# Kernel optimization log

Measured on AMD Instinct MI355X. Metric: run time of the kernel, lower is better.

The kernel has to match this reference:

```python
import jax, jax.numpy as jnp
import numpy as np

N_NODES = 100000
N_EDGES = 1600000
D = 64  # input_dim = hidden_dim = output_dim
EPS = 1e-12


def _sage_layer(x, src, dst, wl, bl, wr, br):
    # gather messages from source nodes: [E, D]
    msg = x[src]
    # scatter-mean onto destination nodes
    s = jax.ops.segment_sum(msg, dst, num_segments=x.shape[0])
    cnt = jax.ops.segment_sum(jnp.ones((src.shape[0], 1), x.dtype), dst, num_segments=x.shape[0])
    prop = s / jnp.maximum(cnt, 1.0)
    out = x @ wl.T + bl + prop @ wr.T + br
    # F.normalize(out, p=2, dim=1)
    norm = jnp.sqrt(jnp.sum(out * out, axis=1, keepdims=True))
    return out / jnp.maximum(norm, EPS)


def setup_inputs() -> dict:
    key = jax.random.key(0)
    ks = jax.random.split(key, 12)
    d = D

    def lin(k, fan_in, fan_out):
        bound = 1.0 / np.sqrt(fan_in)
        kw, kb = jax.random.split(k)
        w = jax.random.uniform(kw, (fan_out, fan_in), jnp.float32, -bound, bound)
        b = jax.random.uniform(kb, (fan_out,), jnp.float32, -bound, bound)
        return w, b

    x = jax.random.normal(ks[0], (N_NODES, d), jnp.float32)
    edge_index = jax.random.randint(ks[1], (2, N_EDGES), 0, N_NODES, jnp.int64)

    w1l, b1l = lin(ks[2], d, d)
    w1r, b1r = lin(ks[3], d, d)
    w2l, b2l = lin(ks[4], d, d)
    w2r, b2r = lin(ks[5], d, d)
    wp1, bp1 = lin(ks[6], d, d)
    wp2, bp2 = lin(ks[7], d, d)

    return {"x": x, "edge_index": edge_index,
            "w1l": w1l, "b1l": b1l, "w1r": w1r, "b1r": b1r,
            "w2l": w2l, "b2l": b2l, "w2r": w2r, "b2r": b2r,
            "wp1": wp1, "bp1": bp1, "wp2": wp2, "bp2": bp2}


def reference(x, edge_index, w1l, b1l, w1r, b1r, w2l, b2l, w2r, b2r, wp1, bp1, wp2, bp2):
    src = edge_index[0]
    dst = edge_index[1]
    # layer 1: GraphSage -> relu (dropout is identity in eval)
    h = _sage_layer(x, src, dst, w1l, b1l, w1r, b1r)
    h = jax.nn.relu(h)
    # layer 2
    h = _sage_layer(h, src, dst, w2l, b2l, w2r, b2r)
    h = jax.nn.relu(h)
    # post_mp: Linear -> Dropout(identity) -> Linear; emb=True so no log_softmax
    h = h @ wp1.T + bp1
    h = h @ wp2.T + bp2
    return h
```

## Files before the change

kernel.cpp:

```cpp
#include <hip/hip_runtime.h>

#define NN 100000
#define NE 1600000
#define DD 64
#define NB 196
#define BKT 512
#define CAP 9000
#define NOCT 12500
#define NH 391
#define NG1 1024

__global__ void init_kernel(int* __restrict__ gcursor) {
  int t = threadIdx.x;
  if (t < NB) gcursor[t] = t * CAP;
}

__launch_bounds__(256)
__global__ void scatter2_kernel(const int* __restrict__ src, const int* __restrict__ dst,
                                int* __restrict__ gcursor, int2* __restrict__ pairs) {
  __shared__ int lh[NB];
  __shared__ int lbase[NB];
  __shared__ int lcur[NB];
  const int NQ = NE / 4;
  int t = blockIdx.x * 256 + threadIdx.x;
  const int nt = NH * 256;
  for (int i = threadIdx.x; i < NB; i += 256) lh[i] = 0;
  __syncthreads();
  int4 dv[4], sv[4];
  bool pv[4];
  #pragma unroll
  for (int k = 0; k < 4; ++k) {
    int idx = t + k * nt;
    pv[k] = idx < NQ;
    if (pv[k]) {
      dv[k] = reinterpret_cast<const int4*>(dst)[idx];
      sv[k] = reinterpret_cast<const int4*>(src)[idx];
      atomicAdd(&lh[dv[k].x >> 9], 1);
      atomicAdd(&lh[dv[k].y >> 9], 1);
      atomicAdd(&lh[dv[k].z >> 9], 1);
      atomicAdd(&lh[dv[k].w >> 9], 1);
    }
  }
  __syncthreads();
  for (int i = threadIdx.x; i < NB; i += 256) {
    lcur[i] = 0;
    lbase[i] = lh[i] ? atomicAdd(&gcursor[i], lh[i]) : 0;
  }
  __syncthreads();
  #pragma unroll
  for (int k = 0; k < 4; ++k) {
    if (pv[k]) {
      int b;
      b = dv[k].x >> 9; pairs[lbase[b] + atomicAdd(&lcur[b], 1)] = make_int2(sv[k].x, dv[k].x);
      b = dv[k].y >> 9; pairs[lbase[b] + atomicAdd(&lcur[b], 1)] = make_int2(sv[k].y, dv[k].y);
      b = dv[k].z >> 9; pairs[lbase[b] + atomicAdd(&lcur[b], 1)] = make_int2(sv[k].z, dv[k].z);
      b = dv[k].w >> 9; pairs[lbase[b] + atomicAdd(&lcur[b], 1)] = make_int2(sv[k].w, dv[k].w);
    }
  }
}

__launch_bounds__(256)
__global__ void csr_kernel(const int2* __restrict__ pairs, const int* __restrict__ gcursor,
                           int* __restrict__ deg, int* __restrict__ off,
                           int* __restrict__ adj) {
  __shared__ int lh[BKT];
  __shared__ int wsum[4];
  int b = blockIdx.x;
  int t = threadIdx.x;
  int rs = b * CAP, re = gcursor[b];
  lh[2 * t] = 0;
  lh[2 * t + 1] = 0;
  __syncthreads();
  for (int i = rs + t; i < re; i += 256)
    atomicAdd(&lh[pairs[i].y - b * BKT], 1);
  __syncthreads();
  int lane = t & 63, w = t >> 6;
  int h0 = lh[2 * t], h1 = lh[2 * t + 1];
  int s = h0 + h1, incl = s;
  #pragma unroll
  for (int o = 1; o < 64; o <<= 1) {
    int u = __shfl_up(incl, o, 64);
    if (lane >= o) incl += u;
  }
  if (lane == 63) wsum[w] = incl;
  __syncthreads();
  int prefix = 0;
  for (int u = 0; u < w; ++u) prefix += wsum[u];
  int excl = prefix + incl - s;
  int n0 = b * BKT + 2 * t, n1 = n0 + 1;
  if (n0 < NN) { deg[n0] = h0; off[n0] = rs + excl; }
  if (n1 < NN) { deg[n1] = h1; off[n1] = rs + excl + h0; }
  lh[2 * t] = excl;
  lh[2 * t + 1] = excl + h0;
  __syncthreads();
  for (int i = rs + t; i < re; i += 256) {
    int2 e = pairs[i];
    int pos = atomicAdd(&lh[e.y - b * BKT], 1);
    adj[rs + pos] = e.x;
  }
}

__launch_bounds__(256)
__global__ void selfgemm_kernel(const float* __restrict__ x,
                                const float* __restrict__ wl,
                                const float* __restrict__ bl,
                                const float* __restrict__ br,
                                float* __restrict__ tmp,
                                const float* __restrict__ wp1, const float* __restrict__ bp1,
                                const float* __restrict__ wp2, const float* __restrict__ bp2,
                                float* __restrict__ wc4f, float* __restrict__ bc) {
  __shared__ float4 wA4[16 * 64] __attribute__((aligned(16)));
  __shared__ float sp[4][8][DD] __attribute__((aligned(16)));
  int bid = blockIdx.x;
  if (bid < NG1) {
    int tid = threadIdx.x;
    int j = tid & 63;
    int w = tid >> 6;
    float* wAf = (float*)wA4;
    for (int i = tid; i < DD * DD; i += 256) {
      int jj = i >> 6, k = i & 63;
      wAf[(((k >> 2) * 64) + jj) * 4 + (k & 3)] = wl[i];
    }
    float bias = bl[j] + br[j];
    __syncthreads();
    const int ngrp = 3125;
    for (int grp = bid; grp < ngrp; grp += NG1) {
      int n0 = (grp * 4 + w) * 8;
      const float4* xg = reinterpret_cast<const float4*>(&x[(size_t)n0 * DD]);
      float4* spv = reinterpret_cast<float4*>(&sp[w][0][0]);
      spv[j] = xg[j];
      spv[j + 64] = xg[j + 64];
      float acc[8];
      #pragma unroll
      for (int i = 0; i < 8; ++i) acc[i] = bias;
      #pragma unroll
      for (int q = 0; q < 16; ++q) {
        int kb = q * 4;
        float4 wq = wA4[q * 64 + j];
        #pragma unroll
        for (int i = 0; i < 8; ++i) {
          float4 sv = *(const float4*)&sp[w][i][kb];
          float a = acc[i];
          a = fmaf(sv.x, wq.x, a);
          a = fmaf(sv.y, wq.y, a);
          a = fmaf(sv.z, wq.z, a);
          a = fmaf(sv.w, wq.w, a);
          acc[i] = a;
        }
      }
      #pragma unroll
      for (int i = 0; i < 8; ++i) tmp[(size_t)(n0 + i) * DD + j] = acc[i];
    }
  } else {
    int t = threadIdx.x;
    for (int idx = t; idx < DD * DD; idx += 256) {
      int jp = idx >> 6, k = idx & 63;
      float s = 0.f;
      #pragma unroll
      for (int m = 0; m < DD; ++m) s = fmaf(wp2[jp * DD + m], wp1[m * DD + k], s);
      wc4f[(((k >> 2) * 64) + jp) * 4 + (k & 3)] = s;
    }
    if (t < DD) {
      float s = bp2[t];
      #pragma unroll
      for (int m = 0; m < DD; ++m) s = fmaf(wp2[t * DD + m], bp1[m], s);
      bc[t] = s;
    }
  }
}

__launch_bounds__(256)
__global__ void gather_kernel(const float* __restrict__ x,
                              const int* __restrict__ off,
                              const int* __restrict__ deg,
                              const int* __restrict__ adj,
                              float* __restrict__ prop) {
  const float4* X = reinterpret_cast<const float4*>(x);
  int wid = (blockIdx.x * 256 + threadIdx.x) >> 6;
  int nwaves = (gridDim.x * 256) >> 6;
  int lane = threadIdx.x & 63;
  int g = lane >> 4;
  int s = lane & 15;
  const int NQUAD = NN / 4;
  for (int q = wid; q < NQUAD; q += nwaves) {
    int n = q * 4 + g;
    int start = off[n];
    int d = deg[n];
    float4 a0 = {0,0,0,0}, a1 = {0,0,0,0}, a2 = {0,0,0,0}, a3 = {0,0,0,0};
    int t = 0;
    for (; t + 4 <= d; t += 4) {
      int i0 = adj[start + t + 0];
      int i1 = adj[start + t + 1];
      int i2 = adj[start + t + 2];
      int i3 = adj[start + t + 3];
      float4 v0 = X[i0 * 16 + s];
      float4 v1 = X[i1 * 16 + s];
      float4 v2 = X[i2 * 16 + s];
      float4 v3 = X[i3 * 16 + s];
      a0.x += v0.x; a0.y += v0.y; a0.z += v0.z; a0.w += v0.w;
      a1.x += v1.x; a1.y += v1.y; a1.z += v1.z; a1.w += v1.w;
      a2.x += v2.x; a2.y += v2.y; a2.z += v2.z; a2.w += v2.w;
      a3.x += v3.x; a3.y += v3.y; a3.z += v3.z; a3.w += v3.w;
    }
    if (t < d) {
      int dm = d - 1;
      int u1 = (t + 1 < d) ? t + 1 : dm;
      int u2 = (t + 2 < d) ? t + 2 : dm;
      int i0 = adj[start + t];
      int i1 = adj[start + u1];
      int i2 = adj[start + u2];
      float4 v0 = X[i0 * 16 + s];
      float4 v1 = X[i1 * 16 + s];
      float4 v2 = X[i2 * 16 + s];
      a0.x += v0.x; a0.y += v0.y; a0.z += v0.z; a0.w += v0.w;
      if (t + 1 < d) { a1.x += v1.x; a1.y += v1.y; a1.z += v1.z; a1.w += v1.w; }
      if (t + 2 < d) { a2.x += v2.x; a2.y += v2.y; a2.z += v2.z; a2.w += v2.w; }
    }
    float rc = 1.0f / fmaxf((float)d, 1.0f);
    float4 r;
    r.x = ((a0.x + a1.x) + (a2.x + a3.x)) * rc;
    r.y = ((a0.y + a1.y) + (a2.y + a3.y)) * rc;
    r.z = ((a0.z + a1.z) + (a2.z + a3.z)) * rc;
    r.w = ((a0.w + a1.w) + (a2.w + a3.w)) * rc;
    reinterpret_cast<float4*>(prop)[n * 16 + s] = r;
  }
}

__launch_bounds__(512, 4)
__global__ void gemm_light_kernel(float* __restrict__ out,
                                  const float* __restrict__ prop,
                                  const float* __restrict__ wr) {
  __shared__ float4 wrA4[16 * 64] __attribute__((aligned(16)));
  __shared__ float pp[8][8][DD] __attribute__((aligned(16)));
  int tid = threadIdx.x;
  int j = tid & 63;
  int w = tid >> 6;
  float* wrf = (float*)wrA4;
  for (int i = tid; i < DD * DD; i += 512) {
    int jj = i >> 6, k = i & 63;
    wrf[(((k >> 2) * 64) + jj) * 4 + (k & 3)] = wr[i];
  }
  __syncthreads();

  const int ngrp = (NOCT + 7) / 8;
  for (int grp = blockIdx.x; grp < ngrp; grp += gridDim.x) {
    int o = grp * 8 + w;
    if (o >= NOCT) continue;
    int n0 = o * 8;

    const float4* pg = reinterpret_cast<const float4*>(&prop[(size_t)n0 * DD]);
    float4* ppv = reinterpret_cast<float4*>(&pp[w][0][0]);
    ppv[j] = pg[j];
    ppv[j + 64] = pg[j + 64];

    float acc[8];
    #pragma unroll
    for (int i = 0; i < 8; ++i) acc[i] = out[(size_t)(n0 + i) * DD + j];

    #pragma unroll
    for (int q = 0; q < 16; ++q) {
      int kb = q * 4;
      float4 wq = wrA4[q * 64 + j];
      #pragma unroll
      for (int i = 0; i < 8; ++i) {
        float4 pv = *(const float4*)&pp[w][i][kb];
        float a = acc[i];
        a = fmaf(pv.x, wq.x, a);
        a = fmaf(pv.y, wq.y, a);
        a = fmaf(pv.z, wq.z, a);
        a = fmaf(pv.w, wq.w, a);
        acc[i] = a;
      }
    }

    #pragma unroll
    for (int i = 0; i < 8; ++i) {
      float a = acc[i];
      float ss = a * a;
      #pragma unroll
      for (int o2 = 32; o2 > 0; o2 >>= 1) ss += __shfl_xor(ss, o2, 64);
      float ov = a / fmaxf(sqrtf(ss), 1e-12f);
      ov = fmaxf(ov, 0.0f);
      out[(size_t)(n0 + i) * DD + j] = ov;
    }
  }
}

__launch_bounds__(512, 4)
__global__ void sage_post_kernel(const float* __restrict__ xin,
                                 const float* __restrict__ prop,
                                 const float* __restrict__ wl,
                                 const float* __restrict__ bl,
                                 const float* __restrict__ wr,
                                 const float* __restrict__ br,
                                 const float4* __restrict__ wc4,
                                 const float* __restrict__ bc,
                                 float* __restrict__ out) {
  __shared__ float4 wlA4[16 * 64] __attribute__((aligned(16)));
  __shared__ float4 wrA4[16 * 64] __attribute__((aligned(16)));
  __shared__ float sp[8][8][DD] __attribute__((aligned(16)));
  __shared__ float pp[8][8][DD] __attribute__((aligned(16)));
  int tid = threadIdx.x;
  int j = tid & 63;
  int w = tid >> 6;

  float* wlf = (float*)wlA4;
  float* wrf = (float*)wrA4;
  for (int i = tid; i < DD * DD; i += 512) {
    int jj = i >> 6, k = i & 63;
    wlf[(((k >> 2) * 64) + jj) * 4 + (k & 3)] = wl[i];
    wrf[(((k >> 2) * 64) + jj) * 4 + (k & 3)] = wr[i];
  }
  float bias = bl[j] + br[j];
  float bcv = bc[j];
  __syncthreads();

  const int ngrp = (NOCT + 7) / 8;
  for (int grp = blockIdx.x; grp < ngrp; grp += gridDim.x) {
    int o = grp * 8 + w;
    if (o >= NOCT) continue;
    int n0 = o * 8;

    const float4* xg = reinterpret_cast<const float4*>(&xin[(size_t)n0 * DD]);
    const float4* pg = reinterpret_cast<const float4*>(&prop[(size_t)n0 * DD]);
    float4* spv = reinterpret_cast<float4*>(&sp[w][0][0]);
    float4* ppv = reinterpret_cast<float4*>(&pp[w][0][0]);
    spv[j] = xg[j];
    spv[j + 64] = xg[j + 64];
    ppv[j] = pg[j];
    ppv[j + 64] = pg[j + 64];

    float acc[8];
    #pragma unroll
    for (int i = 0; i < 8; ++i) acc[i] = bias;

    #pragma unroll
    for (int q = 0; q < 16; ++q) {
      int kb = q * 4;
      float4 wlq = wlA4[q * 64 + j];
      float4 wrq = wrA4[q * 64 + j];
      #pragma unroll
      for (int i = 0; i < 8; ++i) {
        float4 sv = *(const float4*)&sp[w][i][kb];
        float4 pv = *(const float4*)&pp[w][i][kb];
        float a = acc[i];
        a = fmaf(sv.x, wlq.x, a);
        a = fmaf(sv.y, wlq.y, a);
        a = fmaf(sv.z, wlq.z, a);
        a = fmaf(sv.w, wlq.w, a);
        a = fmaf(pv.x, wrq.x, a);
        a = fmaf(pv.y, wrq.y, a);
        a = fmaf(pv.z, wrq.z, a);
        a = fmaf(pv.w, wrq.w, a);
        acc[i] = a;
      }
    }

    #pragma unroll
    for (int i = 0; i < 8; ++i) {
      float a = acc[i];
      float ss = a * a;
      #pragma unroll
      for (int o2 = 32; o2 > 0; o2 >>= 1) ss += __shfl_xor(ss, o2, 64);
      float ov = a / fmaxf(sqrtf(ss), 1e-12f);
      ov = fmaxf(ov, 0.0f);
      sp[w][i][j] = ov;
    }

    float acc2[8];
    #pragma unroll
    for (int i = 0; i < 8; ++i) acc2[i] = bcv;
    #pragma unroll
    for (int q = 0; q < 16; ++q) {
      int kb = q * 4;
      float4 wq = wc4[q * 64 + j];
      #pragma unroll
      for (int i = 0; i < 8; ++i) {
        float4 hv = *(const float4*)&sp[w][i][kb];
        float a = acc2[i];
        a = fmaf(hv.x, wq.x, a);
        a = fmaf(hv.y, wq.y, a);
        a = fmaf(hv.z, wq.z, a);
        a = fmaf(hv.w, wq.w, a);
        acc2[i] = a;
      }
    }
    #pragma unroll
    for (int i = 0; i < 8; ++i) out[(size_t)(n0 + i) * DD + j] = acc2[i];
  }
}

extern "C" void kernel_launch(void* const* d_in, const int* in_sizes, int n_in,
                              void* d_out, int out_size, void* d_ws, size_t ws_size,
                              hipStream_t stream) {
  const float* x   = (const float*)d_in[0];
  const int*   ei  = (const int*)d_in[1];
  const float* w1l = (const float*)d_in[2];
  const float* b1l = (const float*)d_in[3];
  const float* w1r = (const float*)d_in[4];
  const float* b1r = (const float*)d_in[5];
  const float* w2l = (const float*)d_in[6];
  const float* b2l = (const float*)d_in[7];
  const float* w2r = (const float*)d_in[8];
  const float* b2r = (const float*)d_in[9];
  const float* wp1 = (const float*)d_in[10];
  const float* bp1 = (const float*)d_in[11];
  const float* wp2 = (const float*)d_in[12];
  const float* bp2 = (const float*)d_in[13];
  float* out = (float*)d_out;

  const int* src = ei;
  const int* dst = ei + NE;

  int* deg     = (int*)d_ws;
  int* off     = deg + 102400;
  int* aux     = off + 102400;
  int* gcursor = aux;
  float* wc4f  = (float*)(aux + 1024);
  float* bc    = wc4f + 4096;
  int* adj     = (int*)(bc + 1024);
  float* prop  = (float*)(adj + NB * CAP);
  int2* pairs  = (int2*)prop;

  init_kernel<<<1, 256, 0, stream>>>(gcursor);
  scatter2_kernel<<<NH, 256, 0, stream>>>(src, dst, gcursor, pairs);
  csr_kernel<<<NB, 256, 0, stream>>>(pairs, gcursor, deg, off, adj);

  selfgemm_kernel<<<NG1 + 1, 256, 0, stream>>>(x, w1l, b1l, b1r, out,
                                               wp1, bp1, wp2, bp2, wc4f, bc);

  gather_kernel<<<2048, 256, 0, stream>>>(x, off, deg, adj, prop);
  gemm_light_kernel<<<1024, 512, 0, stream>>>(out, prop, w1r);

  gather_kernel<<<2048, 256, 0, stream>>>(out, off, deg, adj, prop);
  sage_post_kernel<<<512, 512, 0, stream>>>(out, prop, w2l, b2l, w2r, b2r,
                                            (const float4*)wc4f, bc, out);
}
```

Measured before the change: 275.9 us.

## Fuse neighbor gather with per-layer GEMM and normalize kernels

Merges each layer's mean-aggregation gather kernel with the following dense transform, normalization and ReLU kernel. Each wave gathers four nodes into shared memory and immediately applies the weight matrices, so the intermediate prop buffer is never written to or read back from global memory. Layer 1 now writes to a separate h buffer, reading the self-term from out, and the second fused kernel reads h and writes the final output. In exchange, the gather's memory latency and the GEMM's arithmetic now run in the same wave, the GEMM tile shrinks from 8 to 4 rows, and the weight staging in shared memory may limit occupancy.

Measured after the change: 302.9 us. +9.8%, slower.

```diff
diff --git a/kernel.cpp b/kernel.cpp
--- a/kernel.cpp
+++ b/kernel.cpp
@@ -6,9 +6,9 @@
 #define NB 196
 #define BKT 512
 #define CAP 9000
-#define NOCT 12500
 #define NH 391
 #define NG1 1024
+#define NQUAD (NN / 4)
 
 __global__ void init_kernel(int* __restrict__ gcursor) {
   int t = threadIdx.x;
@@ -169,19 +169,31 @@
   }
 }
 
-__launch_bounds__(256)
-__global__ void gather_kernel(const float* __restrict__ x,
+__launch_bounds__(512)
+__global__ void fused1_kernel(const float* __restrict__ x,
                               const int* __restrict__ off,
                               const int* __restrict__ deg,
                               const int* __restrict__ adj,
-                              float* __restrict__ prop) {
+                              const float* __restrict__ tmp,
+                              const float* __restrict__ wr,
+                              float* __restrict__ h) {
+  __shared__ float4 wrA4[16 * 64] __attribute__((aligned(16)));
+  __shared__ float pp[8][4][DD] __attribute__((aligned(16)));
+  int tid = threadIdx.x;
+  int j = tid & 63;
+  int w = tid >> 6;
+  float* wrf = (float*)wrA4;
+  for (int i = tid; i < DD * DD; i += 512) {
+    int jj = i >> 6, k = i & 63;
+    wrf[(((k >> 2) * 64) + jj) * 4 + (k & 3)] = wr[i];
+  }
+  __syncthreads();
+
   const float4* X = reinterpret_cast<const float4*>(x);
-  int wid = (blockIdx.x * 256 + threadIdx.x) >> 6;
-  int nwaves = (gridDim.x * 256) >> 6;
-  int lane = threadIdx.x & 63;
-  int g = lane >> 4;
-  int s = lane & 15;
-  const int NQUAD = NN / 4;
+  int g = j >> 4;
+  int s = j & 15;
+  int wid = blockIdx.x * 8 + w;
+  int nwaves = gridDim.x * 8;
   for (int q = wid; q < NQUAD; q += nwaves) {
     int n = q * 4 + g;
     int start = off[n];
@@ -222,47 +234,18 @@
     r.y = ((a0.y + a1.y) + (a2.y + a3.y)) * rc;
     r.z = ((a0.z + a1.z) + (a2.z + a3.z)) * rc;
     r.w = ((a0.w + a1.w) + (a2.w + a3.w)) * rc;
-    reinterpret_cast<float4*>(prop)[n * 16 + s] = r;
-  }
-}
-
-__launch_bounds__(512, 4)
-__global__ void gemm_light_kernel(float* __restrict__ out,
-                                  const float* __restrict__ prop,
-                                  const float* __restrict__ wr) {
-  __shared__ float4 wrA4[16 * 64] __attribute__((aligned(16)));
-  __shared__ float pp[8][8][DD] __attribute__((aligned(16)));
-  int tid = threadIdx.x;
-  int j = tid & 63;
-  int w = tid >> 6;
-  float* wrf = (float*)wrA4;
-  for (int i = tid; i < DD * DD; i += 512) {
-    int jj = i >> 6, k = i & 63;
-    wrf[(((k >> 2) * 64) + jj) * 4 + (k & 3)] = wr[i];
-  }
-  __syncthreads();
-
-  const int ngrp = (NOCT + 7) / 8;
-  for (int grp = blockIdx.x; grp < ngrp; grp += gridDim.x) {
-    int o = grp * 8 + w;
-    if (o >= NOCT) continue;
-    int n0 = o * 8;
-
-    const float4* pg = reinterpret_cast<const float4*>(&prop[(size_t)n0 * DD]);
-    float4* ppv = reinterpret_cast<float4*>(&pp[w][0][0]);
-    ppv[j] = pg[j];
-    ppv[j + 64] = pg[j + 64];
-
-    float acc[8];
-    #pragma unroll
-    for (int i = 0; i < 8; ++i) acc[i] = out[(size_t)(n0 + i) * DD + j];
-
-    #pragma unroll
-    for (int q = 0; q < 16; ++q) {
-      int kb = q * 4;
-      float4 wq = wrA4[q * 64 + j];
-      #pragma unroll
-      for (int i = 0; i < 8; ++i) {
+    *(float4*)&pp[w][g][s * 4] = r;
+
+    int n0 = q * 4;
+    float acc[4];
+    #pragma unroll
+    for (int i = 0; i < 4; ++i) acc[i] = tmp[(size_t)(n0 + i) * DD + j];
+    #pragma unroll
+    for (int qq = 0; qq < 16; ++qq) {
+      int kb = qq * 4;
+      float4 wq = wrA4[qq * 64 + j];
+      #pragma unroll
+      for (int i = 0; i < 4; ++i) {
         float4 pv = *(const float4*)&pp[w][i][kb];
         float a = acc[i];
         a = fmaf(pv.x, wq.x, a);
@@ -272,38 +255,38 @@
         acc[i] = a;
       }
     }
-
-    #pragma unroll
-    for (int i = 0; i < 8; ++i) {
+    #pragma unroll
+    for (int i = 0; i < 4; ++i) {
       float a = acc[i];
       float ss = a * a;
       #pragma unroll
       for (int o2 = 32; o2 > 0; o2 >>= 1) ss += __shfl_xor(ss, o2, 64);
       float ov = a / fmaxf(sqrtf(ss), 1e-12f);
       ov = fmaxf(ov, 0.0f);
-      out[(size_t)(n0 + i) * DD + j] = ov;
-    }
-  }
-}
-
-__launch_bounds__(512, 4)
-__global__ void sage_post_kernel(const float* __restrict__ xin,
-                                 const float* __restrict__ prop,
-                                 const float* __restrict__ wl,
-                                 const float* __restrict__ bl,
-                                 const float* __restrict__ wr,
-                                 const float* __restrict__ br,
-                                 const float4* __restrict__ wc4,
-                                 const float* __restrict__ bc,
-                                 float* __restrict__ out) {
+      h[(size_t)(n0 + i) * DD + j] = ov;
+    }
+  }
+}
+
+__launch_bounds__(512)
+__global__ void fused2_kernel(const float* __restrict__ h,
+                              const int* __restrict__ off,
+                              const int* __restrict__ deg,
+                              const int* __restrict__ adj,
+                              const float* __restrict__ wl,
+                              const float* __restrict__ bl,
+                              const float* __restrict__ wr,
+                              const float* __restrict__ br,
+                              const float4* __restrict__ wc4,
+                              const float* __restrict__ bc,
+                              float* __restrict__ out) {
   __shared__ float4 wlA4[16 * 64] __attribute__((aligned(16)));
   __shared__ float4 wrA4[16 * 64] __attribute__((aligned(16)));
-  __shared__ float sp[8][8][DD] __attribute__((aligned(16)));
-  __shared__ float pp[8][8][DD] __attribute__((aligned(16)));
+  __shared__ float sp[8][4][DD] __attribute__((aligned(16)));
+  __shared__ float pp[8][4][DD] __attribute__((aligned(16)));
   int tid = threadIdx.x;
   int j = tid & 63;
   int w = tid >> 6;
-
   float* wlf = (float*)wlA4;
   float* wrf = (float*)wrA4;
   for (int i = tid; i < DD * DD; i += 512) {
@@ -315,32 +298,68 @@
   float bcv = bc[j];
   __syncthreads();
 
-  const int ngrp = (NOCT + 7) / 8;
-  for (int grp = blockIdx.x; grp < ngrp; grp += gridDim.x) {
-    int o = grp * 8 + w;
-    if (o >= NOCT) continue;
-    int n0 = o * 8;
-
-    const float4* xg = reinterpret_cast<const float4*>(&xin[(size_t)n0 * DD]);
-    const float4* pg = reinterpret_cast<const float4*>(&prop[(size_t)n0 * DD]);
+  const float4* X = reinterpret_cast<const float4*>(h);
+  int g = j >> 4;
+  int s = j & 15;
+  int wid = blockIdx.x * 8 + w;
+  int nwaves = gridDim.x * 8;
+  for (int q = wid; q < NQUAD; q += nwaves) {
+    int n = q * 4 + g;
+    int start = off[n];
+    int d = deg[n];
+    float4 a0 = {0,0,0,0}, a1 = {0,0,0,0}, a2 = {0,0,0,0}, a3 = {0,0,0,0};
+    int t = 0;
+    for (; t + 4 <= d; t += 4) {
+      int i0 = adj[start + t + 0];
+      int i1 = adj[start + t + 1];
+      int i2 = adj[start + t + 2];
+      int i3 = adj[start + t + 3];
+      float4 v0 = X[i0 * 16 + s];
+      float4 v1 = X[i1 * 16 + s];
+      float4 v2 = X[i2 * 16 + s];
+      float4 v3 = X[i3 * 16 + s];
+      a0.x += v0.x; a0.y += v0.y; a0.z += v0.z; a0.w += v0.w;
+      a1.x += v1.x; a1.y += v1.y; a1.z += v1.z; a1.w += v1.w;
+      a2.x += v2.x; a2.y += v2.y; a2.z += v2.z; a2.w += v2.w;
+      a3.x += v3.x; a3.y += v3.y; a3.z += v3.z; a3.w += v3.w;
+    }
+    if (t < d) {
+      int dm = d - 1;
+      int u1 = (t + 1 < d) ? t + 1 : dm;
+      int u2 = (t + 2 < d) ? t + 2 : dm;
+      int i0 = adj[start + t];
+      int i1 = adj[start + u1];
+      int i2 = adj[start + u2];
+      float4 v0 = X[i0 * 16 + s];
+      float4 v1 = X[i1 * 16 + s];
+      float4 v2 = X[i2 * 16 + s];
+      a0.x += v0.x; a0.y += v0.y; a0.z += v0.z; a0.w += v0.w;
+      if (t + 1 < d) { a1.x += v1.x; a1.y += v1.y; a1.z += v1.z; a1.w += v1.w; }
+      if (t + 2 < d) { a2.x += v2.x; a2.y += v2.y; a2.z += v2.z; a2.w += v2.w; }
+    }
+    float rc = 1.0f / fmaxf((float)d, 1.0f);
+    float4 r;
+    r.x = ((a0.x + a1.x) + (a2.x + a3.x)) * rc;
+    r.y = ((a0.y + a1.y) + (a2.y + a3.y)) * rc;
+    r.z = ((a0.z + a1.z) + (a2.z + a3.z)) * rc;
+    r.w = ((a0.w + a1.w) + (a2.w + a3.w)) * rc;
+    *(float4*)&pp[w][g][s * 4] = r;
+
+    int n0 = q * 4;
+    const float4* hg = reinterpret_cast<const float4*>(&h[(size_t)n0 * DD]);
     float4* spv = reinterpret_cast<float4*>(&sp[w][0][0]);
-    float4* ppv = reinterpret_cast<float4*>(&pp[w][0][0]);
-    spv[j] = xg[j];
-    spv[j + 64] = xg[j + 64];
-    ppv[j] = pg[j];
-    ppv[j + 64] = pg[j + 64];
-
-    float acc[8];
-    #pragma unroll
-    for (int i = 0; i < 8; ++i) acc[i] = bias;
-
-    #pragma unroll
-    for (int q = 0; q < 16; ++q) {
-      int kb = q * 4;
-      float4 wlq = wlA4[q * 64 + j];
-      float4 wrq = wrA4[q * 64 + j];
-      #pragma unroll
-      for (int i = 0; i < 8; ++i) {
+    spv[j] = hg[j];
+
+    float acc[4];
+    #pragma unroll
+    for (int i = 0; i < 4; ++i) acc[i] = bias;
+    #pragma unroll
+    for (int qq = 0; qq < 16; ++qq) {
+      int kb = qq * 4;
+      float4 wlq = wlA4[qq * 64 + j];
+      float4 wrq = wrA4[qq * 64 + j];
+      #pragma unroll
+      for (int i = 0; i < 4; ++i) {
         float4 sv = *(const float4*)&sp[w][i][kb];
         float4 pv = *(const float4*)&pp[w][i][kb];
         float a = acc[i];
@@ -357,7 +376,7 @@
     }
 
     #pragma unroll
-    for (int i = 0; i < 8; ++i) {
+    for (int i = 0; i < 4; ++i) {
       float a = acc[i];
       float ss = a * a;
       #pragma unroll
@@ -367,15 +386,15 @@
       sp[w][i][j] = ov;
     }
 
-    float acc2[8];
-    #pragma unroll
-    for (int i = 0; i < 8; ++i) acc2[i] = bcv;
-    #pragma unroll
-    for (int q = 0; q < 16; ++q) {
-      int kb = q * 4;
-      float4 wq = wc4[q * 64 + j];
-      #pragma unroll
-      for (int i = 0; i < 8; ++i) {
+    float acc2[4];
+    #pragma unroll
+    for (int i = 0; i < 4; ++i) acc2[i] = bcv;
+    #pragma unroll
+    for (int qq = 0; qq < 16; ++qq) {
+      int kb = qq * 4;
+      float4 wq = wc4[qq * 64 + j];
+      #pragma unroll
+      for (int i = 0; i < 4; ++i) {
         float4 hv = *(const float4*)&sp[w][i][kb];
         float a = acc2[i];
         a = fmaf(hv.x, wq.x, a);
@@ -386,7 +405,7 @@
       }
     }
     #pragma unroll
-    for (int i = 0; i < 8; ++i) out[(size_t)(n0 + i) * DD + j] = acc2[i];
+    for (int i = 0; i < 4; ++i) out[(size_t)(n0 + i) * DD + j] = acc2[i];
   }
 }
 
@@ -419,8 +438,8 @@
   float* wc4f  = (float*)(aux + 1024);
   float* bc    = wc4f + 4096;
   int* adj     = (int*)(bc + 1024);
-  float* prop  = (float*)(adj + NB * CAP);
-  int2* pairs  = (int2*)prop;
+  float* h     = (float*)(adj + NB * CAP);
+  int2* pairs  = (int2*)h;
 
   init_kernel<<<1, 256, 0, stream>>>(gcursor);
   scatter2_kernel<<<NH, 256, 0, stream>>>(src, dst, gcursor, pairs);
@@ -429,10 +448,8 @@
   selfgemm_kernel<<<NG1 + 1, 256, 0, stream>>>(x, w1l, b1l, b1r, out,
                                                wp1, bp1, wp2, bp2, wc4f, bc);
 
-  gather_kernel<<<2048, 256, 0, stream>>>(x, off, deg, adj, prop);
-  gemm_light_kernel<<<1024, 512, 0, stream>>>(out, prop, w1r);
-
-  gather_kernel<<<2048, 256, 0, stream>>>(out, off, deg, adj, prop);
-  sage_post_kernel<<<512, 512, 0, stream>>>(out, prop, w2l, b2l, w2r, b2r,
-                                            (const float4*)wc4f, bc, out);
-}
+  fused1_kernel<<<2048, 512, 0, stream>>>(x, off, deg, adj, out, w1r, h);
+
+  fused2_kernel<<<1024, 512, 0, stream>>>(h, off, deg, adj, w2l, b2l, w2r, b2r,
+                                          (const float4*)wc4f, bc, out);
+}
```
